# Performance work log

Hardware: AMD Instinct MI355X
Metric: run time of the kernel (lower is better)

The kernel has to match this reference:

```python
import jax, jax.numpy as jnp
import numpy as np

N_POOL = 8  # 'n' from init: pool height factor


def _masked_conv(x, kernel_masked, bias):
    """Pad H,W by 1 with zeros, 3x3 VALID conv whose middle kernel row is zero, ReLU.
    Equivalent to the per-row loop with an explicitly zeroed middle row slice.
    x: [B,H,W,C] NHWC; kernel_masked: [3,3,C,F] (kh=1 row already zeroed)."""
    xp = jnp.pad(x, ((0, 0), (1, 1), (1, 1), (0, 0)))
    y = jax.lax.conv_general_dilated(
        xp, kernel_masked, window_strides=(1, 1), padding='VALID',
        dimension_numbers=('NHWC', 'HWIO', 'NHWC'))
    return jax.nn.relu(y + bias)


def setup_inputs() -> dict:
    key = jax.random.key(0)
    k1, k2, k3 = jax.random.split(key, 3)
    B, H, W, C, F = 8, 512, 512, 16, 16
    feature_map = jax.random.normal(k1, (B, H, W, C), dtype=jnp.float32)
    kernel = jax.random.normal(k2, (3, 3, C, F), dtype=jnp.float32) * 0.1
    bias = jax.random.normal(k3, (F,), dtype=jnp.float32) * 0.01
    return {"feature_map": feature_map, "kernel": kernel, "bias": bias}


def reference(feature_map, kernel, bias):
    B, H, W, C = feature_map.shape
    ph, pw = H // N_POOL, 2
    # AveragePooling2D pool_size=(H/n, 2), strides same, SAME padding (divisible -> exact)
    pooled = feature_map.reshape(B, N_POOL, ph, W // pw, pw, C).mean(axis=(2, 4))  # [B,n,W/2,C]
    # zero the middle kernel row (inpainting: center row of each 3-row window is zeroed)
    row_mask = jnp.array([1.0, 0.0, 1.0], dtype=kernel.dtype)[:, None, None, None]
    kmask = kernel * row_mask
    row_op = _masked_conv(pooled, kmask, bias)                                  # [B,n,W/2,F]
    col_t = _masked_conv(jnp.transpose(pooled, (0, 2, 1, 3)), kmask, bias)      # [B,W/2,n,F]
    col_op = jnp.transpose(col_t, (0, 2, 1, 3))                                  # [B,n,W/2,F]
    F = row_op.shape[-1]
    row_up = jax.image.resize(row_op, (B, H, W, F), method='bilinear')
    col_up = jax.image.resize(col_op, (B, H, W, F), method='bilinear')
    stacked_op = jnp.concatenate([row_up, col_up], axis=3)                       # [B,H,W,2F]
    stacked_orig = jnp.concatenate([feature_map, feature_map], axis=3)           # [B,H,W,2C]
    diff_feature = stacked_orig - stacked_op
    return jnp.concatenate([feature_map, diff_feature], axis=3)                  # [B,H,W,3C]
```

## Files before the change

### kernel.cpp

```cpp
#include <hip/hip_runtime.h>

#define NB 8
#define NH 512
#define NW 512
#define NC 16
#define NPOOL 8
#define NW2 256
#define POOL_ELEMS (NB * NPOOL * NW2 * NC)

__global__ __launch_bounds__(256) void pool_k(const float* __restrict__ fm,
                                              float* __restrict__ pooled) {
  int bid = blockIdx.x;
  int wt = bid & 7;
  int n  = (bid >> 3) & 7;
  int b  = bid >> 6;
  int t = threadIdx.x;
  int wl = t >> 2;
  int cq = t & 3;
  int w = wt * 64 + wl;

  const float* src = fm + ((size_t)((b * NH + n * 64) * NW + w) * NC + cq * 4);
  float4 a = make_float4(0.f, 0.f, 0.f, 0.f);
#pragma unroll 8
  for (int dh = 0; dh < 64; ++dh) {
    float4 v = *(const float4*)(src + (size_t)dh * (NW * NC));
    a.x += v.x; a.y += v.y; a.z += v.z; a.w += v.w;
  }
  a.x += __shfl_xor(a.x, 4);
  a.y += __shfl_xor(a.y, 4);
  a.z += __shfl_xor(a.z, 4);
  a.w += __shfl_xor(a.w, 4);
  if ((t & 4) == 0) {
    int w2 = wt * 32 + (t >> 3);
    const float s = 1.f / 128.f;
    float4 r = make_float4(a.x * s, a.y * s, a.z * s, a.w * s);
    *(float4*)(pooled + ((size_t)((b * NPOOL + n) * NW2 + w2) * NC + cq * 4)) = r;
  }
}

__global__ __launch_bounds__(256) void conv_k(const float* __restrict__ pooled,
                                              const float* __restrict__ kern,
                                              const float* __restrict__ bias,
                                              float* __restrict__ row_op,
                                              float* __restrict__ col_op) {
  int idx = blockIdx.x * 256 + threadIdx.x;
  int f  = idx & 15;
  int w2 = (idx >> 4) & 255;
  int n  = (idx >> 12) & 7;
  int b  = idx >> 15;

  bool nm = n > 0, npv = n < 7, wm = w2 > 0, wp = w2 < 255;
  const float* P = pooled + (size_t)((b * NPOOL + n) * NW2 + w2) * NC;
  const int UP = -NW2 * NC, DN = NW2 * NC, LT = -NC, RT = NC;

  float accR = bias[f];
  float accC = accR;
#pragma unroll
  for (int c = 0; c < 16; ++c) {
    float tl = (nm && wm) ? P[UP + LT + c] : 0.f;
    float tc = nm         ? P[UP + c]      : 0.f;
    float tr = (nm && wp) ? P[UP + RT + c] : 0.f;
    float ml = wm         ? P[LT + c]      : 0.f;
    float mr = wp         ? P[RT + c]      : 0.f;
    float bl = (npv && wm) ? P[DN + LT + c] : 0.f;
    float bc = npv         ? P[DN + c]      : 0.f;
    float br = (npv && wp) ? P[DN + RT + c] : 0.f;

    float k00 = kern[((0 * 3 + 0) * 16 + c) * 16 + f];
    float k01 = kern[((0 * 3 + 1) * 16 + c) * 16 + f];
    float k02 = kern[((0 * 3 + 2) * 16 + c) * 16 + f];
    float k20 = kern[((2 * 3 + 0) * 16 + c) * 16 + f];
    float k21 = kern[((2 * 3 + 1) * 16 + c) * 16 + f];
    float k22 = kern[((2 * 3 + 2) * 16 + c) * 16 + f];

    accR += tl * k00 + tc * k01 + tr * k02 + bl * k20 + bc * k21 + br * k22;
    accC += tl * k00 + ml * k01 + bl * k02 + tr * k20 + mr * k21 + br * k22;
  }
  row_op[idx] = fmaxf(accR, 0.f);
  col_op[idx] = fmaxf(accC, 0.f);
}

__global__ __launch_bounds__(256) void out_k(const float* __restrict__ fm,
                                             const float* __restrict__ row_op,
                                             const float* __restrict__ col_op,
                                             float* __restrict__ out) {
  __shared__ float lds[64 * 48];
  int bid = blockIdx.x;
  int wt = bid & 7;
  int h  = (bid >> 3) & 511;
  int b  = bid >> 12;
  int t = threadIdx.x;
  int pl = t >> 2;
  int cq = t & 3;
  int w = wt * 64 + pl;

  float x  = (h + 0.5f) * (1.f / 64.f) - 0.5f;
  float xf = floorf(x);
  float wx = x - xf;
  int n0  = (int)xf;
  int n0c = n0 < 0 ? 0 : n0;
  int n1c = (n0 + 1 > 7) ? 7 : n0 + 1;

  float y  = (w + 0.5f) * 0.5f - 0.5f;
  float yf = floorf(y);
  float wy = y - yf;
  int y0  = (int)yf;
  int y0c = y0 < 0 ? 0 : y0;
  int y1c = (y0 + 1 > 255) ? 255 : y0 + 1;

  float w00 = (1.f - wx) * (1.f - wy);
  float w01 = (1.f - wx) * wy;
  float w10 = wx * (1.f - wy);
  float w11 = wx * wy;

  size_t rowbase = (size_t)(b * NH + h) * NW;
  float4 fv = *(const float4*)(fm + (rowbase + w) * NC + cq * 4);

  const float* R  = row_op + (size_t)b * (NPOOL * NW2 * NC);
  const float* Cl = col_op + (size_t)b * (NPOOL * NW2 * NC);
#define TAP(A, nn, yy) (*(const float4*)((A) + ((size_t)(nn) * NW2 + (yy)) * NC + cq * 4))
  float4 r00 = TAP(R, n0c, y0c), r01 = TAP(R, n0c, y1c);
  float4 r10 = TAP(R, n1c, y0c), r11 = TAP(R, n1c, y1c);
  float4 c00 = TAP(Cl, n0c, y0c), c01 = TAP(Cl, n0c, y1c);
  float4 c10 = TAP(Cl, n1c, y0c), c11 = TAP(Cl, n1c, y1c);
#undef TAP

  float4 rup, cup;
  rup.x = w00 * r00.x + w01 * r01.x + w10 * r10.x + w11 * r11.x;
  rup.y = w00 * r00.y + w01 * r01.y + w10 * r10.y + w11 * r11.y;
  rup.z = w00 * r00.z + w01 * r01.z + w10 * r10.z + w11 * r11.z;
  rup.w = w00 * r00.w + w01 * r01.w + w10 * r10.w + w11 * r11.w;
  cup.x = w00 * c00.x + w01 * c01.x + w10 * c10.x + w11 * c11.x;
  cup.y = w00 * c00.y + w01 * c01.y + w10 * c10.y + w11 * c11.y;
  cup.z = w00 * c00.z + w01 * c01.z + w10 * c10.z + w11 * c11.z;
  cup.w = w00 * c00.w + w01 * c01.w + w10 * c10.w + w11 * c11.w;

  float* L = lds + pl * 48 + cq * 4;
  L[0]  = fv.x;          L[1]  = fv.y;          L[2]  = fv.z;          L[3]  = fv.w;
  L[16] = fv.x - rup.x;  L[17] = fv.y - rup.y;  L[18] = fv.z - rup.z;  L[19] = fv.w - rup.w;
  L[32] = fv.x - cup.x;  L[33] = fv.y - cup.y;  L[34] = fv.z - cup.z;  L[35] = fv.w - cup.w;
  __syncthreads();

  float* obase = out + ((size_t)(b * NH + h) * NW + wt * 64) * 48;
#pragma unroll
  for (int k = 0; k < 3; ++k) {
    int i = t + k * 256;
    *(float4*)(obase + (size_t)i * 4) = *(const float4*)(lds + i * 4);
  }
}

extern "C" void kernel_launch(void* const* d_in, const int* in_sizes, int n_in,
                              void* d_out, int out_size, void* d_ws, size_t ws_size,
                              hipStream_t stream) {
  const float* fm   = (const float*)d_in[0];
  const float* kern = (const float*)d_in[1];
  const float* bias = (const float*)d_in[2];
  float* out = (float*)d_out;

  float* pooled = (float*)d_ws;
  float* row_op = pooled + POOL_ELEMS;
  float* col_op = row_op + POOL_ELEMS;

  pool_k<<<NB * NPOOL * 8, 256, 0, stream>>>(fm, pooled);
  conv_k<<<POOL_ELEMS / 256, 256, 0, stream>>>(pooled, kern, bias, row_op, col_op);
  out_k<<<NB * NH * (NW / 64), 256, 0, stream>>>(fm, row_op, col_op, out);
}
```

Before: 529.2 us.

## Split pooling rows across 1024 threads, vectorize conv loads, nontemporal output stores

The pooling kernel now launches 1024 threads per block. Each group of 256 threads sums 16 of the 64 rows, and the partial sums are combined through shared memory. This raises memory-level parallelism, since the earlier 512-block launch had too few waves to saturate bandwidth. The conv kernel now loads neighbour pixels as float4 instead of scalar loads. The output kernel uses nontemporal stores so the large output bypasses cache retention. Together these add a block-wide barrier and more registers per block in exchange.

```diff
diff --git a/kernel.cpp b/kernel.cpp
--- a/kernel.cpp
+++ b/kernel.cpp
@@ -8,33 +8,48 @@
 #define NW2 256
 #define POOL_ELEMS (NB * NPOOL * NW2 * NC)
 
-__global__ __launch_bounds__(256) void pool_k(const float* __restrict__ fm,
-                                              float* __restrict__ pooled) {
+typedef float vf4 __attribute__((ext_vector_type(4)));
+
+__global__ __launch_bounds__(1024) void pool_k(const float* __restrict__ fm,
+                                               float* __restrict__ pooled) {
+  __shared__ float4 part[3][256];
   int bid = blockIdx.x;
   int wt = bid & 7;
   int n  = (bid >> 3) & 7;
   int b  = bid >> 6;
-  int t = threadIdx.x;
-  int wl = t >> 2;
-  int cq = t & 3;
+  int t  = threadIdx.x;
+  int rg = t >> 8;
+  int tt = t & 255;
+  int wl = tt >> 2;
+  int cq = tt & 3;
   int w = wt * 64 + wl;
 
-  const float* src = fm + ((size_t)((b * NH + n * 64) * NW + w) * NC + cq * 4);
+  const float* src =
+      fm + ((size_t)((b * NH + n * 64 + rg * 16) * NW + w) * NC + cq * 4);
   float4 a = make_float4(0.f, 0.f, 0.f, 0.f);
-#pragma unroll 8
-  for (int dh = 0; dh < 64; ++dh) {
+#pragma unroll
+  for (int dh = 0; dh < 16; ++dh) {
     float4 v = *(const float4*)(src + (size_t)dh * (NW * NC));
     a.x += v.x; a.y += v.y; a.z += v.z; a.w += v.w;
   }
-  a.x += __shfl_xor(a.x, 4);
-  a.y += __shfl_xor(a.y, 4);
-  a.z += __shfl_xor(a.z, 4);
-  a.w += __shfl_xor(a.w, 4);
-  if ((t & 4) == 0) {
-    int w2 = wt * 32 + (t >> 3);
-    const float s = 1.f / 128.f;
-    float4 r = make_float4(a.x * s, a.y * s, a.z * s, a.w * s);
-    *(float4*)(pooled + ((size_t)((b * NPOOL + n) * NW2 + w2) * NC + cq * 4)) = r;
+  if (rg) part[rg - 1][tt] = a;
+  __syncthreads();
+  if (rg == 0) {
+    float4 p0 = part[0][tt], p1 = part[1][tt], p2 = part[2][tt];
+    a.x += p0.x + p1.x + p2.x;
+    a.y += p0.y + p1.y + p2.y;
+    a.z += p0.z + p1.z + p2.z;
+    a.w += p0.w + p1.w + p2.w;
+    a.x += __shfl_xor(a.x, 4);
+    a.y += __shfl_xor(a.y, 4);
+    a.z += __shfl_xor(a.z, 4);
+    a.w += __shfl_xor(a.w, 4);
+    if ((tt & 4) == 0) {
+      int w2 = wt * 32 + (tt >> 3);
+      const float s = 1.f / 128.f;
+      float4 r = make_float4(a.x * s, a.y * s, a.z * s, a.w * s);
+      *(float4*)(pooled + ((size_t)((b * NPOOL + n) * NW2 + w2) * NC + cq * 4)) = r;
+    }
   }
 }
 
@@ -49,32 +64,39 @@
   int n  = (idx >> 12) & 7;
   int b  = idx >> 15;
 
-  bool nm = n > 0, npv = n < 7, wm = w2 > 0, wp = w2 < 255;
+  bool nm = n > 0, np = n < 7, wm = w2 > 0, wp = w2 < 255;
   const float* P = pooled + (size_t)((b * NPOOL + n) * NW2 + w2) * NC;
   const int UP = -NW2 * NC, DN = NW2 * NC, LT = -NC, RT = NC;
+  const float4 z = make_float4(0.f, 0.f, 0.f, 0.f);
 
   float accR = bias[f];
   float accC = accR;
 #pragma unroll
-  for (int c = 0; c < 16; ++c) {
-    float tl = (nm && wm) ? P[UP + LT + c] : 0.f;
-    float tc = nm         ? P[UP + c]      : 0.f;
-    float tr = (nm && wp) ? P[UP + RT + c] : 0.f;
-    float ml = wm         ? P[LT + c]      : 0.f;
-    float mr = wp         ? P[RT + c]      : 0.f;
-    float bl = (npv && wm) ? P[DN + LT + c] : 0.f;
-    float bc = npv         ? P[DN + c]      : 0.f;
-    float br = (npv && wp) ? P[DN + RT + c] : 0.f;
-
-    float k00 = kern[((0 * 3 + 0) * 16 + c) * 16 + f];
-    float k01 = kern[((0 * 3 + 1) * 16 + c) * 16 + f];
-    float k02 = kern[((0 * 3 + 2) * 16 + c) * 16 + f];
-    float k20 = kern[((2 * 3 + 0) * 16 + c) * 16 + f];
-    float k21 = kern[((2 * 3 + 1) * 16 + c) * 16 + f];
-    float k22 = kern[((2 * 3 + 2) * 16 + c) * 16 + f];
-
-    accR += tl * k00 + tc * k01 + tr * k02 + bl * k20 + bc * k21 + br * k22;
-    accC += tl * k00 + ml * k01 + bl * k02 + tr * k20 + mr * k21 + br * k22;
+  for (int q = 0; q < 4; ++q) {
+    float4 tl = (nm && wm) ? *(const float4*)(P + UP + LT + q * 4) : z;
+    float4 tc = nm         ? *(const float4*)(P + UP + q * 4)      : z;
+    float4 tr = (nm && wp) ? *(const float4*)(P + UP + RT + q * 4) : z;
+    float4 ml = wm         ? *(const float4*)(P + LT + q * 4)      : z;
+    float4 mr = wp         ? *(const float4*)(P + RT + q * 4)      : z;
+    float4 bl = (np && wm) ? *(const float4*)(P + DN + LT + q * 4) : z;
+    float4 bc = np         ? *(const float4*)(P + DN + q * 4)      : z;
+    float4 br = (np && wp) ? *(const float4*)(P + DN + RT + q * 4) : z;
+#pragma unroll
+    for (int j = 0; j < 4; ++j) {
+      int c = q * 4 + j;
+      float k00 = kern[((0 * 3 + 0) * 16 + c) * 16 + f];
+      float k01 = kern[((0 * 3 + 1) * 16 + c) * 16 + f];
+      float k02 = kern[((0 * 3 + 2) * 16 + c) * 16 + f];
+      float k20 = kern[((2 * 3 + 0) * 16 + c) * 16 + f];
+      float k21 = kern[((2 * 3 + 1) * 16 + c) * 16 + f];
+      float k22 = kern[((2 * 3 + 2) * 16 + c) * 16 + f];
+      float tlj = ((const float*)&tl)[j], tcj = ((const float*)&tc)[j];
+      float trj = ((const float*)&tr)[j], mlj = ((const float*)&ml)[j];
+      float mrj = ((const float*)&mr)[j], blj = ((const float*)&bl)[j];
+      float bcj = ((const float*)&bc)[j], brj = ((const float*)&br)[j];
+      accR += tlj * k00 + tcj * k01 + trj * k02 + blj * k20 + bcj * k21 + brj * k22;
+      accC += tlj * k00 + mlj * k01 + blj * k02 + trj * k20 + mrj * k21 + brj * k22;
+    }
   }
   row_op[idx] = fmaxf(accR, 0.f);
   col_op[idx] = fmaxf(accC, 0.f);
@@ -145,7 +167,8 @@
 #pragma unroll
   for (int k = 0; k < 3; ++k) {
     int i = t + k * 256;
-    *(float4*)(obase + (size_t)i * 4) = *(const float4*)(lds + i * 4);
+    vf4 v = *(const vf4*)(lds + i * 4);
+    __builtin_nontemporal_store(v, (vf4*)(obase + (size_t)i * 4));
   }
 }
 
@@ -161,7 +184,7 @@
   float* row_op = pooled + POOL_ELEMS;
   float* col_op = row_op + POOL_ELEMS;
 
-  pool_k<<<NB * NPOOL * 8, 256, 0, stream>>>(fm, pooled);
+  pool_k<<<NB * NPOOL * 8, 1024, 0, stream>>>(fm, pooled);
   conv_k<<<POOL_ELEMS / 256, 256, 0, stream>>>(pooled, kern, bias, row_op, col_op);
   out_k<<<NB * NH * (NW / 64), 256, 0, stream>>>(fm, row_op, col_op, out);
 }
```

New measurement: 505.2 us. 1.05x faster.
